# Kernel tuning notes

Measured on AMD Instinct MI355X. Metric: run time of the kernel, lower is better.

## Reference

```python
import math
import jax, jax.numpy as jnp
import numpy as np

R, C, B, E = 64, 256, 4, 768
Q, QD = 256, 512
H = 12
D = E // H

def setup_inputs() -> dict:
    key = jax.random.key(0)
    ks = jax.random.split(key, 10)
    def lin(kw, out_d, in_d):
        s = 1.0 / math.sqrt(in_d)
        return jax.random.uniform(kw, (out_d, in_d), jnp.float32, -s, s)
    return {
        "x": jax.random.normal(ks[0], (R, C, B, E), jnp.float32),
        "query": jax.random.normal(ks[1], (Q, B, QD), jnp.float32),
        "Wq": lin(ks[2], E, QD), "bq": jnp.zeros((E,), jnp.float32),
        "Wk": lin(ks[3], E, E), "bk": jnp.zeros((E,), jnp.float32),
        "Wv": lin(ks[4], E, E), "bv": jnp.zeros((E,), jnp.float32),
        "Wo": lin(ks[5], E, E), "bo": jnp.zeros((E,), jnp.float32),
    }

def reference(x, query, Wq, bq, Wk, bk, Wv, bv, Wo, bo):
    # x: (R, C, B, E) rows/cols/batch/embed; query: (Q, B, QD)
    q_cols = query.shape[0]
    scaling = (D ** -0.5) / math.sqrt(q_cols)  # align_scaling over query rows
    q = (query @ Wq.T + bq).reshape(q_cols, B, H, D) * scaling  # (Q,B,H,D)
    k = (x @ Wk.T + bk).reshape(R, C, B, H, D)
    # tied row attention: scores summed over the column axis c
    attn = jnp.einsum("qnhd,rcnhd->hnqr", q, k)  # (H,B,Q,R)
    probs = jax.nn.softmax(attn, axis=-1)
    v = (x @ Wv.T + bv).reshape(R, C, B, H, D)
    # value update: sum attn over query cols q, broadcast over c
    ctx = jnp.einsum("hnqr,rcnhd->rcnhd", probs, v).reshape(R, C, B, E)
    out = ctx @ Wo.T + bo  # (R,C,B,E)
    return out
```

## Files before the change

kernel.cpp:

```cpp
#include <hip/hip_runtime.h>
#include <hip/hip_bf16.h>


typedef __attribute__((ext_vector_type(8))) short bf16x8;
typedef __attribute__((ext_vector_type(4))) float f32x4;

__device__ __forceinline__ void load_lds16(const void* g, void* l) {
    __builtin_amdgcn_global_load_lds(
        (const __attribute__((address_space(1))) void*)g,
        (__attribute__((address_space(3))) void*)l, 16, 0, 0);
}

__global__ __launch_bounds__(256) void xsum_cvt_kernel(const float* __restrict__ x,
                                                       float* __restrict__ xsp,
                                                       __hip_bfloat16* __restrict__ xb) {
    int gid = blockIdx.x * 256 + threadIdx.x;
    int e4 = gid % 192;
    int t2 = gid / 192;
    int rb = t2 & 255;
    int part = t2 >> 8;
    int r = rb >> 2, n = rb & 3;
    size_t base = (size_t)r * 786432 + (size_t)part * 196608 + n * 768 + e4 * 4;
    const float4* px = (const float4*)(x + base);
    ushort* xbu = (ushort*)xb + base;
    float4 s = {0.f, 0.f, 0.f, 0.f};
    #pragma unroll 4
    for (int c = 0; c < 64; ++c) {
        float4 v = px[(size_t)c * 768];
        s.x += v.x; s.y += v.y; s.z += v.z; s.w += v.w;
        union { ushort4 u; __hip_bfloat16 h[4]; } pk;
        pk.h[0] = __float2bfloat16(v.x); pk.h[1] = __float2bfloat16(v.y);
        pk.h[2] = __float2bfloat16(v.z); pk.h[3] = __float2bfloat16(v.w);
        *(ushort4*)(xbu + (size_t)c * 3072) = pk.u;
    }
    *(float4*)(xsp + (size_t)part * 196608 + rb * 768 + e4 * 4) = s;
}

__global__ __launch_bounds__(256) void f2b_kernel(const float* __restrict__ in,
                                                  __hip_bfloat16* __restrict__ out, int n4) {
    int i = blockIdx.x * 256 + threadIdx.x;
    if (i < n4) {
        float4 v = ((const float4*)in)[i];
        out[i * 4 + 0] = __float2bfloat16(v.x);
        out[i * 4 + 1] = __float2bfloat16(v.y);
        out[i * 4 + 2] = __float2bfloat16(v.z);
        out[i * 4 + 3] = __float2bfloat16(v.w);
    }
}

template <int MODE>
__global__ __launch_bounds__(256) void gemm_kernel(const float* __restrict__ A,
                                                   const float* __restrict__ W,
                                                   const float* __restrict__ bias,
                                                   float* __restrict__ Cf,
                                                   int M, int N, int K, float p0) {
    __shared__ float As[16][65];
    __shared__ float Ws[16][65];
    int tid = threadIdx.x;
    int tx = tid & 15, ty = tid >> 4;
    int m0 = blockIdx.y * 64, n0 = blockIdx.x * 64;
    float acc[4][4] = {};

    for (int k0 = 0; k0 < K; k0 += 16) {
        #pragma unroll
        for (int i = 0; i < 4; ++i) {
            int idx = tid + 256 * i;
            int mm = idx >> 4, kk = idx & 15;
            size_t ai = (size_t)(m0 + mm) * K + k0 + kk;
            if (MODE == 0)
                As[kk][mm] = A[ai] + A[ai + 196608] + A[ai + 393216] + A[ai + 589824];
            else
                As[kk][mm] = A[ai];
            Ws[kk][mm] = W[(size_t)(n0 + mm) * K + k0 + kk];
        }
        __syncthreads();
        #pragma unroll
        for (int kk = 0; kk < 16; ++kk) {
            float a[4], b[4];
            #pragma unroll
            for (int i = 0; i < 4; ++i) a[i] = As[kk][ty + 16 * i];
            #pragma unroll
            for (int j = 0; j < 4; ++j) b[j] = Ws[kk][tx + 16 * j];
            #pragma unroll
            for (int i = 0; i < 4; ++i)
                #pragma unroll
                for (int j = 0; j < 4; ++j) acc[i][j] += a[i] * b[j];
        }
        __syncthreads();
    }
    #pragma unroll
    for (int i = 0; i < 4; ++i) {
        int m = m0 + ty + 16 * i;
        #pragma unroll
        for (int j = 0; j < 4; ++j) {
            int n = n0 + tx + 16 * j;
            float v = acc[i][j];
            if (MODE == 0) Cf[(size_t)m * N + n] = v + p0 * bias[n];
            else           Cf[(size_t)m * N + n] = (v + bias[n]) * p0;
        }
    }
}

__global__ __launch_bounds__(256) void attn_kernel(const float* __restrict__ qp,
                                                   const float* __restrict__ ksum,
                                                   float* __restrict__ psum) {
    int h = blockIdx.x >> 2;
    int n = blockIdx.x & 3;
    __shared__ float kd[64][65];
    __shared__ float sacc[4][64];
    int tid = threadIdx.x;

    #pragma unroll
    for (int it = 0; it < 16; ++it) {
        int idx = tid + 256 * it;
        int r = idx >> 6, d = idx & 63;
        kd[r][d] = ksum[(size_t)(r * 4 + n) * 768 + h * 64 + d];
    }
    __syncthreads();

    int wave = tid >> 6, lane = tid & 63;
    float acc = 0.f;
    for (int q = wave; q < 256; q += 4) {
        float qv = qp[(size_t)(q * 4 + n) * 768 + h * 64 + lane];
        float val = 0.f;
        #pragma unroll
        for (int d = 0; d < 64; ++d) val += __shfl(qv, d) * kd[lane][d];
        float mx = val;
        #pragma unroll
        for (int off = 1; off < 64; off <<= 1) mx = fmaxf(mx, __shfl_xor(mx, off));
        float p = __expf(val - mx);
        float s = p;
        #pragma unroll
        for (int off = 1; off < 64; off <<= 1) s += __shfl_xor(s, off);
        acc += p / s;
    }
    sacc[wave][lane] = acc;
    __syncthreads();
    if (tid < 64) {
        psum[blockIdx.x * 64 + tid] =
            sacc[0][tid] + sacc[1][tid] + sacc[2][tid] + sacc[3][tid];
    }
}


__device__ __forceinline__ int swz(int R, int kg) {
    return ((R >> 1) << 6) + ((((((R & 1) << 2) | kg)) ^ ((R >> 1) & 7)) << 3);
}

template <int MODE>
__global__ __launch_bounds__(512, 2) void mfma_gemm2(const ushort* __restrict__ A,
                                                     const ushort* __restrict__ W,
                                                     const float* __restrict__ bias,
                                                     const float* __restrict__ scale,
                                                     float* __restrict__ Cf,
                                                     __hip_bfloat16* __restrict__ Cb,
                                                     int M, int N, int K) {
    __shared__ short lds[49152];
    const int NT = K >> 5;
    int tid = threadIdx.x;
    int wave = tid >> 6, lane = tid & 63;
    int wr = wave >> 2, wc = wave & 3;
    int r16 = lane & 15, kg = lane >> 4;

    int cpx = gridDim.x >> 3;
    int h = blockIdx.x;
    int orig = (h & 7) * cpx + (h >> 3);
    int nbx = N >> 8;
    int by = orig / nbx, bx = orig - by * nbx;
    int m0 = by << 8, n0 = bx << 8;

    int c0 = tid, c1 = tid + 512;
    int p0c = c0 >> 3, s0c = (c0 & 7) ^ (p0c & 7);
    int row0 = (p0c << 1) | (s0c >> 2), kg0 = s0c & 3;
    int p1c = c1 >> 3, s1c = (c1 & 7) ^ (p1c & 7);
    int row1 = (p1c << 1) | (s1c >> 2), kg1 = s1c & 3;
    const ushort* pA0 = A + (size_t)(m0 + row0) * K + kg0 * 8;
    const ushort* pA1 = A + (size_t)(m0 + row1) * K + kg1 * 8;
    const ushort* pB0 = W + (size_t)(n0 + row0) * K + kg0 * 8;
    const ushort* pB1 = W + (size_t)(n0 + row1) * K + kg1 * 8;
    int dep0 = (wave * 64) * 8;
    int dep1 = (512 + wave * 64) * 8;

    f32x4 acc[8][4];
    #pragma unroll
    for (int i = 0; i < 8; ++i)
        #pragma unroll
        for (int j = 0; j < 4; ++j) acc[i][j] = (f32x4){0.f, 0.f, 0.f, 0.f};

    load_lds16(pA0 + 0, &lds[dep0]);
    load_lds16(pA1 + 0, &lds[dep1]);
    load_lds16(pB0 + 0, &lds[8192 + dep0]);
    load_lds16(pB1 + 0, &lds[8192 + dep1]);
    load_lds16(pA0 + 32, &lds[16384 + dep0]);
    load_lds16(pA1 + 32, &lds[16384 + dep1]);
    load_lds16(pB0 + 32, &lds[16384 + 8192 + dep0]);
    load_lds16(pB1 + 32, &lds[16384 + 8192 + dep1]);

    int s = 0;
    int s2b = 2 * 16384;
    int k2 = 64;
    for (int t = 0; t < NT; ++t) {
        if (t + 1 < NT) { asm volatile("s_waitcnt vmcnt(4)" ::: "memory"); }
        else           { asm volatile("s_waitcnt vmcnt(0)" ::: "memory"); }
        __builtin_amdgcn_s_barrier();
        __builtin_amdgcn_sched_barrier(0);
        const short* sb = &lds[s * 16384];

        bf16x8 bv[4], af[4];
        #pragma unroll
        for (int ni = 0; ni < 4; ++ni)
            bv[ni] = *(const bf16x8*)&sb[8192 + swz(wc * 64 + ni * 16 + r16, kg)];
        #pragma unroll
        for (int mi = 0; mi < 4; ++mi)
            af[mi] = *(const bf16x8*)&sb[swz(wr * 128 + mi * 16 + r16, kg)];
        if (t + 2 < NT) {
            load_lds16(pA0 + k2, &lds[s2b + dep0]);
            load_lds16(pA1 + k2, &lds[s2b + dep1]);
        }
        __builtin_amdgcn_s_setprio(1);
        #pragma unroll
        for (int mi = 0; mi < 4; ++mi)
            #pragma unroll
            for (int ni = 0; ni < 4; ++ni)
                acc[mi][ni] = __builtin_amdgcn_mfma_f32_16x16x32_bf16(
                    af[mi], bv[ni], acc[mi][ni], 0, 0, 0);
        __builtin_amdgcn_s_setprio(0);

        #pragma unroll
        for (int mi = 0; mi < 4; ++mi)
            af[mi] = *(const bf16x8*)&sb[swz(wr * 128 + 64 + mi * 16 + r16, kg)];
        if (t + 2 < NT) {
            load_lds16(pB0 + k2, &lds[s2b + 8192 + dep0]);
            load_lds16(pB1 + k2, &lds[s2b + 8192 + dep1]);
        }
        __builtin_amdgcn_s_setprio(1);
        #pragma unroll
        for (int mi = 0; mi < 4; ++mi)
            #pragma unroll
            for (int ni = 0; ni < 4; ++ni)
                acc[4 + mi][ni] = __builtin_amdgcn_mfma_f32_16x16x32_bf16(
                    af[mi], bv[ni], acc[4 + mi][ni], 0, 0, 0);
        __builtin_amdgcn_s_setprio(0);

        s = (s == 2) ? 0 : s + 1;
        s2b = (s2b == 2 * 16384) ? 0 : s2b + 16384;
        k2 += 32;
    }

    int col = lane & 15, rbase = (lane >> 4) << 2;
    #pragma unroll
    for (int ni = 0; ni < 4; ++ni) {
        int gn = n0 + wc * 64 + ni * 16 + col;
        float bn = bias[gn];
        #pragma unroll
        for (int mi = 0; mi < 8; ++mi) {
            int gmb = m0 + wr * 128 + mi * 16 + rbase;
            #pragma unroll
            for (int i = 0; i < 4; ++i) {
                int gm = gmb + i;
                float v = acc[mi][ni][i] + bn;
                if (MODE == 2) {
                    float sc = scale[(((gn >> 6) << 2) + (gm & 3)) * 64 + (gm >> 10)];
                    Cb[(size_t)gm * N + gn] = __float2bfloat16(v * sc);
                } else {
                    Cf[(size_t)gm * N + gn] = v;
                }
            }
        }
    }
}

extern "C" void kernel_launch(void* const* d_in, const int* in_sizes, int n_in,
                              void* d_out, int out_size, void* d_ws, size_t ws_size,
                              hipStream_t stream) {
    const float* x     = (const float*)d_in[0];
    const float* query = (const float*)d_in[1];
    const float* Wq    = (const float*)d_in[2];
    const float* bq    = (const float*)d_in[3];
    const float* Wk    = (const float*)d_in[4];
    const float* bk    = (const float*)d_in[5];
    const float* Wv    = (const float*)d_in[6];
    const float* bv    = (const float*)d_in[7];
    const float* Wo    = (const float*)d_in[8];
    const float* bo    = (const float*)d_in[9];
    float* out = (float*)d_out;

    __hip_bfloat16* xb   = (__hip_bfloat16*)d_ws;
    __hip_bfloat16* vtmp = xb + 50331648;
    __hip_bfloat16* Wvb  = vtmp + 50331648;
    __hip_bfloat16* Wob  = Wvb + 589824;
    float* xsum = (float*)(Wob + 589824);
    float* ksum = xsum + 196608;
    float* qp   = ksum + 196608;
    float* psum = qp + 786432;
    float* xsp = (float*)vtmp;

    xsum_cvt_kernel<<<768, 256, 0, stream>>>(x, xsp, xb);
    f2b_kernel<<<576, 256, 0, stream>>>(Wv, Wvb, 147456);
    f2b_kernel<<<576, 256, 0, stream>>>(Wo, Wob, 147456);
    gemm_kernel<0><<<dim3(12, 4), 256, 0, stream>>>(xsp, Wk, bk, ksum, 256, 768, 768, 256.0f);
    gemm_kernel<1><<<dim3(12, 16), 256, 0, stream>>>(query, Wq, bq, qp, 1024, 768, 512, 0.0078125f);
    attn_kernel<<<48, 256, 0, stream>>>(qp, ksum, psum);
    mfma_gemm2<2><<<768, 512, 0, stream>>>(
        (const ushort*)xb, (const ushort*)Wvb, bv, psum, nullptr, vtmp, 65536, 768, 768);
    mfma_gemm2<3><<<768, 512, 0, stream>>>(
        (const ushort*)vtmp, (const ushort*)Wob, bo, nullptr, out, nullptr, 65536, 768, 768);
}
```

Before: 738.5 us.

## Fuse prep kernels, split-K small GEMMs, deepen MFMA GEMM pipeline to four stages

After: 677.8 us. -8.2%, faster.

```diff
diff --git a/kernel.cpp b/kernel.cpp
--- a/kernel.cpp
+++ b/kernel.cpp
@@ -11,40 +11,44 @@
         (__attribute__((address_space(3))) void*)l, 16, 0, 0);
 }
 
-__global__ __launch_bounds__(256) void xsum_cvt_kernel(const float* __restrict__ x,
-                                                       float* __restrict__ xsp,
-                                                       __hip_bfloat16* __restrict__ xb) {
-    int gid = blockIdx.x * 256 + threadIdx.x;
-    int e4 = gid % 192;
-    int t2 = gid / 192;
-    int rb = t2 & 255;
-    int part = t2 >> 8;
-    int r = rb >> 2, n = rb & 3;
-    size_t base = (size_t)r * 786432 + (size_t)part * 196608 + n * 768 + e4 * 4;
-    const float4* px = (const float4*)(x + base);
-    ushort* xbu = (ushort*)xb + base;
-    float4 s = {0.f, 0.f, 0.f, 0.f};
-    #pragma unroll 4
-    for (int c = 0; c < 64; ++c) {
-        float4 v = px[(size_t)c * 768];
-        s.x += v.x; s.y += v.y; s.z += v.z; s.w += v.w;
-        union { ushort4 u; __hip_bfloat16 h[4]; } pk;
-        pk.h[0] = __float2bfloat16(v.x); pk.h[1] = __float2bfloat16(v.y);
-        pk.h[2] = __float2bfloat16(v.z); pk.h[3] = __float2bfloat16(v.w);
-        *(ushort4*)(xbu + (size_t)c * 3072) = pk.u;
-    }
-    *(float4*)(xsp + (size_t)part * 196608 + rb * 768 + e4 * 4) = s;
-}
-
-__global__ __launch_bounds__(256) void f2b_kernel(const float* __restrict__ in,
-                                                  __hip_bfloat16* __restrict__ out, int n4) {
-    int i = blockIdx.x * 256 + threadIdx.x;
-    if (i < n4) {
-        float4 v = ((const float4*)in)[i];
-        out[i * 4 + 0] = __float2bfloat16(v.x);
-        out[i * 4 + 1] = __float2bfloat16(v.y);
-        out[i * 4 + 2] = __float2bfloat16(v.z);
-        out[i * 4 + 3] = __float2bfloat16(v.w);
+__global__ __launch_bounds__(256) void prep_kernel(const float* __restrict__ x,
+                                                   float* __restrict__ xsp,
+                                                   __hip_bfloat16* __restrict__ xb,
+                                                   const float* __restrict__ Wv,
+                                                   __hip_bfloat16* __restrict__ Wvb,
+                                                   const float* __restrict__ Wo,
+                                                   __hip_bfloat16* __restrict__ Wob) {
+    int b = blockIdx.x, tid = threadIdx.x;
+    if (b < 768) {
+        int gid = b * 256 + tid;
+        int e4 = gid % 192;
+        int t2 = gid / 192;
+        int rb = t2 & 255;
+        int part = t2 >> 8;
+        int r = rb >> 2, n = rb & 3;
+        size_t base = (size_t)r * 786432 + (size_t)part * 196608 + n * 768 + e4 * 4;
+        const float4* px = (const float4*)(x + base);
+        ushort* xbu = (ushort*)xb + base;
+        float4 s = {0.f, 0.f, 0.f, 0.f};
+        #pragma unroll 4
+        for (int c = 0; c < 64; ++c) {
+            float4 v = px[(size_t)c * 768];
+            s.x += v.x; s.y += v.y; s.z += v.z; s.w += v.w;
+            union { ushort4 u; __hip_bfloat16 h[4]; } pk;
+            pk.h[0] = __float2bfloat16(v.x); pk.h[1] = __float2bfloat16(v.y);
+            pk.h[2] = __float2bfloat16(v.z); pk.h[3] = __float2bfloat16(v.w);
+            *(ushort4*)(xbu + (size_t)c * 3072) = pk.u;
+        }
+        *(float4*)(xsp + (size_t)part * 196608 + rb * 768 + e4 * 4) = s;
+    } else {
+        const float* src = (b < 1344) ? Wv : Wo;
+        __hip_bfloat16* dst = (b < 1344) ? Wvb : Wob;
+        int i = (b - ((b < 1344) ? 768 : 1344)) * 256 + tid;
+        float4 v = ((const float4*)src)[i];
+        dst[i * 4 + 0] = __float2bfloat16(v.x);
+        dst[i * 4 + 1] = __float2bfloat16(v.y);
+        dst[i * 4 + 2] = __float2bfloat16(v.z);
+        dst[i * 4 + 3] = __float2bfloat16(v.w);
     }
 }
 
@@ -53,15 +57,17 @@
                                                    const float* __restrict__ W,
                                                    const float* __restrict__ bias,
                                                    float* __restrict__ Cf,
-                                                   int M, int N, int K, float p0) {
+                                                   int M, int N, int K, int KS, float p0) {
     __shared__ float As[16][65];
     __shared__ float Ws[16][65];
     int tid = threadIdx.x;
     int tx = tid & 15, ty = tid >> 4;
     int m0 = blockIdx.y * 64, n0 = blockIdx.x * 64;
+    int z = blockIdx.z;
+    int kbeg = z * KS, kend = kbeg + KS;
     float acc[4][4] = {};
 
-    for (int k0 = 0; k0 < K; k0 += 16) {
+    for (int k0 = kbeg; k0 < kend; k0 += 16) {
         #pragma unroll
         for (int i = 0; i < 4; ++i) {
             int idx = tid + 256 * i;
@@ -88,6 +94,7 @@
         }
         __syncthreads();
     }
+    float* Cz = Cf + (size_t)z * M * N;
     #pragma unroll
     for (int i = 0; i < 4; ++i) {
         int m = m0 + ty + 16 * i;
@@ -95,8 +102,8 @@
         for (int j = 0; j < 4; ++j) {
             int n = n0 + tx + 16 * j;
             float v = acc[i][j];
-            if (MODE == 0) Cf[(size_t)m * N + n] = v + p0 * bias[n];
-            else           Cf[(size_t)m * N + n] = (v + bias[n]) * p0;
+            if (MODE == 0) Cz[(size_t)m * N + n] = v + ((z == 0) ? p0 * bias[n] : 0.f);
+            else           Cz[(size_t)m * N + n] = (v + ((z == 0) ? bias[n] : 0.f)) * p0;
         }
     }
 }
@@ -106,7 +113,8 @@
                                                    float* __restrict__ psum) {
     int h = blockIdx.x >> 2;
     int n = blockIdx.x & 3;
-    __shared__ float kd[64][65];
+    __shared__ float kd[64][68];
+    __shared__ float qs[4][68];
     __shared__ float sacc[4][64];
     int tid = threadIdx.x;
 
@@ -114,17 +122,24 @@
     for (int it = 0; it < 16; ++it) {
         int idx = tid + 256 * it;
         int r = idx >> 6, d = idx & 63;
-        kd[r][d] = ksum[(size_t)(r * 4 + n) * 768 + h * 64 + d];
+        size_t ki = (size_t)(r * 4 + n) * 768 + h * 64 + d;
+        kd[r][d] = ksum[ki] + ksum[ki + 196608] + ksum[ki + 393216] + ksum[ki + 589824];
     }
     __syncthreads();
 
     int wave = tid >> 6, lane = tid & 63;
     float acc = 0.f;
     for (int q = wave; q < 256; q += 4) {
-        float qv = qp[(size_t)(q * 4 + n) * 768 + h * 64 + lane];
+        size_t qi = (size_t)(q * 4 + n) * 768 + h * 64 + lane;
+        float qv = qp[qi] + qp[qi + 786432];
+        qs[wave][lane] = qv;
         float val = 0.f;
         #pragma unroll
-        for (int d = 0; d < 64; ++d) val += __shfl(qv, d) * kd[lane][d];
+        for (int d4 = 0; d4 < 16; ++d4) {
+            float4 kv = *(const float4*)&kd[lane][d4 * 4];
+            float4 qq = *(const float4*)&qs[wave][d4 * 4];
+            val += qq.x * kv.x + qq.y * kv.y + qq.z * kv.z + qq.w * kv.w;
+        }
         float mx = val;
         #pragma unroll
         for (int off = 1; off < 64; off <<= 1) mx = fmaxf(mx, __shfl_xor(mx, off));
@@ -155,7 +170,7 @@
                                                      float* __restrict__ Cf,
                                                      __hip_bfloat16* __restrict__ Cb,
                                                      int M, int N, int K) {
-    __shared__ short lds[49152];
+    __shared__ short lds[65536];
     const int NT = K >> 5;
     int tid = threadIdx.x;
     int wave = tid >> 6, lane = tid & 63;
@@ -163,8 +178,8 @@
     int r16 = lane & 15, kg = lane >> 4;
 
     int cpx = gridDim.x >> 3;
-    int h = blockIdx.x;
-    int orig = (h & 7) * cpx + (h >> 3);
+    int hh = blockIdx.x;
+    int orig = (hh & 7) * cpx + (hh >> 3);
     int nbx = N >> 8;
     int by = orig / nbx, bx = orig - by * nbx;
     int m0 = by << 8, n0 = bx << 8;
@@ -187,24 +202,24 @@
         #pragma unroll
         for (int j = 0; j < 4; ++j) acc[i][j] = (f32x4){0.f, 0.f, 0.f, 0.f};
 
-    load_lds16(pA0 + 0, &lds[dep0]);
-    load_lds16(pA1 + 0, &lds[dep1]);
-    load_lds16(pB0 + 0, &lds[8192 + dep0]);
-    load_lds16(pB1 + 0, &lds[8192 + dep1]);
-    load_lds16(pA0 + 32, &lds[16384 + dep0]);
-    load_lds16(pA1 + 32, &lds[16384 + dep1]);
-    load_lds16(pB0 + 32, &lds[16384 + 8192 + dep0]);
-    load_lds16(pB1 + 32, &lds[16384 + 8192 + dep1]);
-
-    int s = 0;
-    int s2b = 2 * 16384;
-    int k2 = 64;
+    #pragma unroll
+    for (int p = 0; p < 3; ++p) {
+        int sb = p * 16384, ko = p * 32;
+        load_lds16(pA0 + ko, &lds[sb + dep0]);
+        load_lds16(pA1 + ko, &lds[sb + dep1]);
+        load_lds16(pB0 + ko, &lds[sb + 8192 + dep0]);
+        load_lds16(pB1 + ko, &lds[sb + 8192 + dep1]);
+    }
+
     for (int t = 0; t < NT; ++t) {
-        if (t + 1 < NT) { asm volatile("s_waitcnt vmcnt(4)" ::: "memory"); }
-        else           { asm volatile("s_waitcnt vmcnt(0)" ::: "memory"); }
+        if (t + 2 < NT)      { asm volatile("s_waitcnt vmcnt(8)" ::: "memory"); }
+        else if (t + 1 < NT) { asm volatile("s_waitcnt vmcnt(4)" ::: "memory"); }
+        else                 { asm volatile("s_waitcnt vmcnt(0)" ::: "memory"); }
         __builtin_amdgcn_s_barrier();
         __builtin_amdgcn_sched_barrier(0);
-        const short* sb = &lds[s * 16384];
+        const short* sb = &lds[(t & 3) * 16384];
+        int s3 = ((t + 3) & 3) * 16384;
+        int k3 = (t + 3) * 32;
 
         bf16x8 bv[4], af[4];
         #pragma unroll
@@ -213,9 +228,9 @@
         #pragma unroll
         for (int mi = 0; mi < 4; ++mi)
             af[mi] = *(const bf16x8*)&sb[swz(wr * 128 + mi * 16 + r16, kg)];
-        if (t + 2 < NT) {
-            load_lds16(pA0 + k2, &lds[s2b + dep0]);
-            load_lds16(pA1 + k2, &lds[s2b + dep1]);
+        if (t + 3 < NT) {
+            load_lds16(pA0 + k3, &lds[s3 + dep0]);
+            load_lds16(pA1 + k3, &lds[s3 + dep1]);
         }
         __builtin_amdgcn_s_setprio(1);
         #pragma unroll
@@ -229,9 +244,9 @@
         #pragma unroll
         for (int mi = 0; mi < 4; ++mi)
             af[mi] = *(const bf16x8*)&sb[swz(wr * 128 + 64 + mi * 16 + r16, kg)];
-        if (t + 2 < NT) {
-            load_lds16(pB0 + k2, &lds[s2b + 8192 + dep0]);
-            load_lds16(pB1 + k2, &lds[s2b + 8192 + dep1]);
+        if (t + 3 < NT) {
+            load_lds16(pB0 + k3, &lds[s3 + 8192 + dep0]);
+            load_lds16(pB1 + k3, &lds[s3 + 8192 + dep1]);
         }
         __builtin_amdgcn_s_setprio(1);
         #pragma unroll
@@ -241,10 +256,6 @@
                 acc[4 + mi][ni] = __builtin_amdgcn_mfma_f32_16x16x32_bf16(
                     af[mi], bv[ni], acc[4 + mi][ni], 0, 0, 0);
         __builtin_amdgcn_s_setprio(0);
-
-        s = (s == 2) ? 0 : s + 1;
-        s2b = (s2b == 2 * 16384) ? 0 : s2b + 16384;
-        k2 += 32;
     }
 
     int col = lane & 15, rbase = (lane >> 4) << 2;
@@ -289,17 +300,14 @@
     __hip_bfloat16* vtmp = xb + 50331648;
     __hip_bfloat16* Wvb  = vtmp + 50331648;
     __hip_bfloat16* Wob  = Wvb + 589824;
-    float* xsum = (float*)(Wob + 589824);
-    float* ksum = xsum + 196608;
-    float* qp   = ksum + 196608;
-    float* psum = qp + 786432;
+    float* ksum = (float*)(Wob + 589824);
+    float* qp   = ksum + 786432;
+    float* psum = qp + 1572864;
     float* xsp = (float*)vtmp;
 
-    xsum_cvt_kernel<<<768, 256, 0, stream>>>(x, xsp, xb);
-    f2b_kernel<<<576, 256, 0, stream>>>(Wv, Wvb, 147456);
-    f2b_kernel<<<576, 256, 0, stream>>>(Wo, Wob, 147456);
-    gemm_kernel<0><<<dim3(12, 4), 256, 0, stream>>>(xsp, Wk, bk, ksum, 256, 768, 768, 256.0f);
-    gemm_kernel<1><<<dim3(12, 16), 256, 0, stream>>>(query, Wq, bq, qp, 1024, 768, 512, 0.0078125f);
+    prep_kernel<<<1920, 256, 0, stream>>>(x, xsp, xb, Wv, Wvb, Wo, Wob);
+    gemm_kernel<0><<<dim3(12, 4, 4), 256, 0, stream>>>(xsp, Wk, bk, ksum, 256, 768, 768, 192, 256.0f);
+    gemm_kernel<1><<<dim3(12, 16, 2), 256, 0, stream>>>(query, Wq, bq, qp, 1024, 768, 512, 256, 0.0078125f);
     attn_kernel<<<48, 256, 0, stream>>>(qp, ksum, psum);
     mfma_gemm2<2><<<768, 512, 0, stream>>>(
         (const ushort*)xb, (const ushort*)Wvb, bv, psum, nullptr, vtmp, 65536, 768, 768);
```
